# Optimization experiments

Measured on AMD Instinct MI355X. Metric: run time of the kernel, lower is better.

## Reference

```python
import jax, jax.numpy as jnp
import numpy as np

NUM_GRAPHS = 512
NODES_PER_GRAPH = 200  # == N_rois
EDGES_PER_GRAPH = 3200  # avg degree 16
N_ROIS = 200
HIDDEN = 64
OUT = 2


def setup_inputs() -> dict:
    key = jax.random.key(0)
    ks = jax.random.split(key, 7)
    N = NUM_GRAPHS * NODES_PER_GRAPH
    E = NUM_GRAPHS * EDGES_PER_GRAPH
    x = jax.random.normal(ks[0], (N, N_ROIS), dtype=jnp.float32)
    # edges sampled within each graph's node block
    base = jnp.repeat(jnp.arange(NUM_GRAPHS, dtype=jnp.int64) * NODES_PER_GRAPH, EDGES_PER_GRAPH)
    local = jax.random.randint(ks[1], (2, E), 0, NODES_PER_GRAPH, dtype=jnp.int64)
    edge_index = local + base[None, :]
    batch = jnp.arange(N, dtype=jnp.int64) // NODES_PER_GRAPH
    conv_w = jax.random.normal(ks[2], (N_ROIS, HIDDEN), dtype=jnp.float32) * 0.1
    conv_b = jax.random.normal(ks[3], (HIDDEN,), dtype=jnp.float32) * 0.1
    lin_w = jax.random.normal(ks[4], (HIDDEN, OUT), dtype=jnp.float32) * 0.1
    lin_b = jax.random.normal(ks[5], (OUT,), dtype=jnp.float32) * 0.1
    return {"x": x, "edge_index": edge_index, "batch": batch,
            "conv_w": conv_w, "conv_b": conv_b, "lin_w": lin_w, "lin_b": lin_b}


def reference(x, edge_index, batch, conv_w, conv_b, lin_w, lin_b):
    N = x.shape[0]
    # GCNConv: linear transform first (N_rois -> hidden), then normalized aggregation
    h = x @ conv_w  # [N, H]
    loops = jnp.arange(N, dtype=edge_index.dtype)
    src = jnp.concatenate([edge_index[0], loops])  # add self-loops (PyG default)
    dst = jnp.concatenate([edge_index[1], loops])
    deg = jax.ops.segment_sum(jnp.ones_like(dst, dtype=h.dtype), dst, num_segments=N)
    dinv = jnp.where(deg > 0, jax.lax.rsqrt(deg), jnp.zeros_like(deg))
    norm = dinv[src] * dinv[dst]  # D^-1/2 (A+I) D^-1/2 edge weights
    agg = jax.ops.segment_sum(h[src] * norm[:, None], dst, num_segments=N) + conv_b
    hr = jax.nn.relu(agg)
    x_pool = jax.ops.segment_max(hr, batch, num_segments=NUM_GRAPHS)  # [G, H]
    out = x_pool @ lin_w + lin_b  # [G, OUT]
    return out, x_pool
```

## Files before the change

### kernel.cpp

```cpp
#include <hip/hip_runtime.h>

#define NUM_GRAPHS 512
#define NPG 200
#define EPG 3200
#define NROIS 200
#define HID 64
#define OUTC 2
#define NT (NUM_GRAPHS * NPG)
#define APITCH 232
#define HPITCH 232
#define WIMG_ELEMS (7 * 4 * 2 * 64 * 8)
#define WS_NEEDED ((size_t)WIMG_ELEMS * 2 + (size_t)HID * NT * 2)

typedef short v8s __attribute__((ext_vector_type(8)));
typedef float v4f __attribute__((ext_vector_type(4)));

__device__ __forceinline__ unsigned bf16_rne(float f) {
  unsigned u = __float_as_uint(f);
  return (u + 0x7fffu + ((u >> 16) & 1u)) >> 16;
}

__global__ void prep_wimg(const float* __restrict__ cw, unsigned short* __restrict__ wimg) {
  int idx = blockIdx.x * 256 + threadIdx.x;
  if (idx >= WIMG_ELEMS) return;
  int i    = idx & 7;
  int lane = (idx >> 3) & 63;
  int hl   = (idx >> 9) & 1;
  int nt   = (idx >> 10) & 3;
  int kt   = idx >> 12;
  int k  = kt * 32 + (lane >> 4) * 8 + i;
  int ch = nt * 16 + (lane & 15);
  float f = (k < NROIS) ? cw[k * HID + ch] : 0.f;
  unsigned hi = bf16_rne(f);
  float lo = f - __uint_as_float(hi << 16);
  wimg[idx] = hl ? (unsigned short)(__float_as_uint(lo) >> 16) : (unsigned short)hi;
}

struct __align__(16) Smem1 {
  unsigned short xhi[64 * HPITCH];
  unsigned short xlo[64 * HPITCH];
};

__global__ __launch_bounds__(256, 2)
void gcn_gemm1(const float* __restrict__ x,
               const unsigned short* __restrict__ wimg,
               unsigned short* __restrict__ hpT) {
  __shared__ Smem1 s;
  const int tid = threadIdx.x;
  const int blk = blockIdx.x;
  const int lane = tid & 63;
  const int w = __builtin_amdgcn_readfirstlane(tid >> 6);
  const int ml = tid & 15;
  const int q  = (tid >> 4) & 3;

  #pragma unroll
  for (int t = 0; t < 13; ++t) {
    int i = tid + t * 256;
    if (i < 3200) {
      int node = i / 50;
      int kc = (i - node * 50) * 4;
      const float4 v = *(const float4*)(x + (size_t)(blk * 64 + node) * NROIS + kc);
      const float ff[4] = {v.x, v.y, v.z, v.w};
      unsigned hh[4], ll[4];
      #pragma unroll
      for (int e = 0; e < 4; ++e) {
        unsigned u = __float_as_uint(ff[e]);
        hh[e] = u >> 16;
        float lo = ff[e] - __uint_as_float(hh[e] << 16);
        ll[e] = __float_as_uint(lo) >> 16;
      }
      uint2 ph = {hh[0] | (hh[1] << 16), hh[2] | (hh[3] << 16)};
      uint2 pl = {ll[0] | (ll[1] << 16), ll[2] | (ll[3] << 16)};
      *(uint2*)&s.xhi[node * HPITCH + kc] = ph;
      *(uint2*)&s.xlo[node * HPITCH + kc] = pl;
    }
  }
  for (int i = tid; i < 64 * 32; i += 256) {
    int node = i >> 5, c = 200 + (i & 31);
    s.xhi[node * HPITCH + c] = 0;
    s.xlo[node * HPITCH + c] = 0;
  }
  __syncthreads();

  v4f acc[4];
  #pragma unroll
  for (int nt = 0; nt < 4; ++nt) acc[nt] = (v4f){0.f, 0.f, 0.f, 0.f};

  for (int kt = 0; kt < 7; ++kt) {
    const int k0 = kt * 32 + q * 8;
    const v8s xh = *(const v8s*)&s.xhi[(w * 16 + ml) * HPITCH + k0];
    const v8s xl = *(const v8s*)&s.xlo[(w * 16 + ml) * HPITCH + k0];
    #pragma unroll
    for (int nt = 0; nt < 4; ++nt) {
      const unsigned short* pw = wimg + (size_t)(((kt * 4 + nt) * 2) * 64 + lane) * 8;
      const v8s whi = *(const v8s*)pw;
      const v8s wlo = *(const v8s*)(pw + 64 * 8);
      acc[nt] = __builtin_amdgcn_mfma_f32_16x16x32_bf16(whi, xl, acc[nt], 0, 0, 0);
      acc[nt] = __builtin_amdgcn_mfma_f32_16x16x32_bf16(wlo, xh, acc[nt], 0, 0, 0);
      acc[nt] = __builtin_amdgcn_mfma_f32_16x16x32_bf16(whi, xh, acc[nt], 0, 0, 0);
    }
  }

  const int gnode = blk * 64 + w * 16 + ml;
  #pragma unroll
  for (int nt = 0; nt < 4; ++nt) {
    #pragma unroll
    for (int r = 0; r < 4; ++r) {
      const int ch = nt * 16 + q * 4 + r;
      hpT[(size_t)ch * NT + gnode] = (unsigned short)bf16_rne(acc[nt][r]);
    }
  }
}

struct __align__(16) Smem2 {
  unsigned char adj[208 * APITCH];
  unsigned short hpTl[HID * HPITCH];
  float dinv[NPG];
  int cnt[NPG];
  int pool[HID];
};

__global__ __launch_bounds__(512, 4)
void gcn_agg(const int* __restrict__ ei,
             const unsigned short* __restrict__ hpT,
             const float* __restrict__ cb,
             const float* __restrict__ lw,
             const float* __restrict__ lb,
             float* __restrict__ out,
             int Etot) {
  __shared__ Smem2 s;
  const int g = blockIdx.x;
  const int tid = threadIdx.x;
  const int base = g * NPG;
  const int ebase = g * EPG;
  const int lane = tid & 63;
  const int w = __builtin_amdgcn_readfirstlane(tid >> 6);
  const int ml = tid & 15;
  const int q  = (tid >> 4) & 3;

  {
    uint4* z = (uint4*)&s;
    const uint4 z4 = {0u, 0u, 0u, 0u};
    #pragma unroll
    for (int i = 0; i < 10; ++i) {
      int idx = tid + i * 512;
      if (idx < (208 * APITCH + HID * HPITCH * 2) / 16) z[idx] = z4;
    }
    if (tid < NPG) s.cnt[tid] = 0;
    if (tid < HID) s.pool[tid] = 0;
  }
  __syncthreads();

  int esrc[7], edst[7];
  #pragma unroll
  for (int r = 0; r < 7; ++r) {
    int e = tid + r * 512;
    esrc[r] = -1; edst[r] = 0;
    if (e < EPG) {
      esrc[r] = ei[ebase + e] - base;
      edst[r] = ei[Etot + ebase + e] - base;
      atomicAdd(&s.cnt[edst[r]], 1);
    }
  }
  __syncthreads();

  if (tid < NPG) s.dinv[tid] = rsqrtf((float)(s.cnt[tid] + 1));
  __syncthreads();

  {
    unsigned* adjW = (unsigned*)s.adj;
    #pragma unroll
    for (int r = 0; r < 7; ++r) {
      if (esrc[r] >= 0) {
        int idx = edst[r] * APITCH + esrc[r];
        atomicAdd(&adjW[idx >> 2], 1u << ((idx & 3) * 8));
      }
    }
    if (tid < NPG) {
      int idx = tid * APITCH + tid;
      atomicAdd(&adjW[idx >> 2], 1u << ((idx & 3) * 8));
    }
  }

  #pragma unroll
  for (int t = 0; t < 13; ++t) {
    int i = tid + t * 512;
    if (i < HID * 100) {
      int ch = i / 100;
      int c2 = (i - ch * 100) * 2;
      unsigned v = *(const unsigned*)(hpT + (size_t)ch * NT + base + c2);
      float f0 = __uint_as_float(v << 16)         * s.dinv[c2];
      float f1 = __uint_as_float(v & 0xffff0000u) * s.dinv[c2 + 1];
      *(unsigned*)&s.hpTl[ch * HPITCH + c2] = bf16_rne(f0) | (bf16_rne(f1) << 16);
    }
  }
  __syncthreads();

  {
    int mts[2];
    mts[0] = w;
    mts[1] = (w < 5) ? 8 + w : -1;

    v4f acc2[2][4];
    #pragma unroll
    for (int a = 0; a < 2; ++a)
      #pragma unroll
      for (int b = 0; b < 4; ++b)
        acc2[a][b] = (v4f){0.f, 0.f, 0.f, 0.f};

    for (int kt = 0; kt < 7; ++kt) {
      const int k0 = kt * 32 + q * 8;

      v8s bf[4];
      #pragma unroll
      for (int nt = 0; nt < 4; ++nt)
        bf[nt] = *(const v8s*)&s.hpTl[(nt * 16 + ml) * HPITCH + k0];

      #pragma unroll
      for (int mi = 0; mi < 2; ++mi) {
        if (mts[mi] >= 0) {
          const int row = mts[mi] * 16 + ml;
          const uint2 dd = *(const uint2*)&s.adj[row * APITCH + k0];
          v8s af;
          #pragma unroll
          for (int i = 0; i < 4; ++i) {
            af[i]     = (short)(__float_as_uint((float)((dd.x >> (8 * i)) & 0xffu)) >> 16);
            af[i + 4] = (short)(__float_as_uint((float)((dd.y >> (8 * i)) & 0xffu)) >> 16);
          }
          #pragma unroll
          for (int nt = 0; nt < 4; ++nt)
            acc2[mi][nt] = __builtin_amdgcn_mfma_f32_16x16x32_bf16(af, bf[nt], acc2[mi][nt], 0, 0, 0);
        }
      }
    }

    float cbv[4];
    #pragma unroll
    for (int nt = 0; nt < 4; ++nt) cbv[nt] = cb[nt * 16 + ml];
    float mx[4] = {0.f, 0.f, 0.f, 0.f};
    #pragma unroll
    for (int mi = 0; mi < 2; ++mi) {
      if (mts[mi] >= 0) {
        #pragma unroll
        for (int r = 0; r < 4; ++r) {
          const int row = mts[mi] * 16 + q * 4 + r;
          if (row < NPG) {
            const float dv = s.dinv[row];
            #pragma unroll
            for (int nt = 0; nt < 4; ++nt) {
              float v = fmaxf(fmaf(dv, acc2[mi][nt][r], cbv[nt]), 0.f);
              mx[nt] = fmaxf(mx[nt], v);
            }
          }
        }
      }
    }
    #pragma unroll
    for (int nt = 0; nt < 4; ++nt) {
      mx[nt] = fmaxf(mx[nt], __shfl_xor(mx[nt], 16));
      mx[nt] = fmaxf(mx[nt], __shfl_xor(mx[nt], 32));
    }
    if (q == 0 && (lane >> 5) == 0) {
      #pragma unroll
      for (int nt = 0; nt < 4; ++nt)
        atomicMax(&s.pool[nt * 16 + ml], __float_as_int(mx[nt]));
    }
  }
  __syncthreads();

  if (tid < HID) {
    const float xp = __int_as_float(s.pool[tid]);
    out[NUM_GRAPHS * OUTC + g * HID + tid] = xp;
    float p0 = xp * lw[tid * 2 + 0];
    float p1 = xp * lw[tid * 2 + 1];
    #pragma unroll
    for (int off = 32; off > 0; off >>= 1) {
      p0 += __shfl_down(p0, off);
      p1 += __shfl_down(p1, off);
    }
    if (tid == 0) {
      out[g * OUTC + 0] = p0 + lb[0];
      out[g * OUTC + 1] = p1 + lb[1];
    }
  }
}

struct __align__(16) SmemF {
  unsigned char adj[208 * APITCH];
  unsigned short hpT[HID * HPITCH];
  float dinv[NPG];
  int cnt[NPG];
  int pool[HID];
};

__global__ __launch_bounds__(512, 4)
void gcn_fused_fb(const float* __restrict__ x,
                  const int* __restrict__ ei,
                  const float* __restrict__ cw,
                  const float* __restrict__ cb,
                  const float* __restrict__ lw,
                  const float* __restrict__ lb,
                  float* __restrict__ out,
                  int Etot) {
  __shared__ SmemF s;
  const int g = blockIdx.x;
  const int tid = threadIdx.x;
  const int base = g * NPG;
  const int ebase = g * EPG;
  const int lane = tid & 63;
  const int w = __builtin_amdgcn_readfirstlane(tid >> 6);
  const int ml = tid & 15;
  const int q  = (tid >> 4) & 3;

  {
    uint4* z = (uint4*)&s;
    const uint4 z4 = {0u, 0u, 0u, 0u};
    #pragma unroll
    for (int i = 0; i < 10; ++i) {
      int idx = tid + i * 512;
      if (idx < (208 * APITCH + HID * HPITCH * 2) / 16) z[idx] = z4;
    }
    if (tid < NPG) s.cnt[tid] = 0;
    if (tid < HID) s.pool[tid] = 0;
  }
  __syncthreads();

  int esrc[7], edst[7];
  #pragma unroll
  for (int r = 0; r < 7; ++r) {
    int e = tid + r * 512;
    esrc[r] = -1; edst[r] = 0;
    if (e < EPG) {
      esrc[r] = ei[ebase + e] - base;
      edst[r] = ei[Etot + ebase + e] - base;
      atomicAdd(&s.cnt[edst[r]], 1);
    }
  }
  __syncthreads();

  if (tid < NPG) s.dinv[tid] = rsqrtf((float)(s.cnt[tid] + 1));

  {
    unsigned* adjW = (unsigned*)s.adj;
    #pragma unroll
    for (int r = 0; r < 7; ++r) {
      if (esrc[r] >= 0) {
        int idx = edst[r] * APITCH + esrc[r];
        atomicAdd(&adjW[idx >> 2], 1u << ((idx & 3) * 8));
      }
    }
    if (tid < NPG) {
      int idx = tid * APITCH + tid;
      atomicAdd(&adjW[idx >> 2], 1u << ((idx & 3) * 8));
    }
  }
  __syncthreads();

  {
    int mts[2];
    mts[0] = w;
    mts[1] = (w < 5) ? 8 + w : -1;
    v4f acc[2][4];
    #pragma unroll
    for (int a = 0; a < 2; ++a)
      #pragma unroll
      for (int b = 0; b < 4; ++b)
        acc[a][b] = (v4f){0.f, 0.f, 0.f, 0.f};

    for (int kt = 0; kt < 7; ++kt) {
      const int k0 = kt * 32 + q * 8;
      const bool kok = (k0 < NROIS);
      v8s bhi[4], blo[4];
      #pragma unroll
      for (int nt = 0; nt < 4; ++nt) {
        #pragma unroll
        for (int i = 0; i < 8; ++i) {
          float f = kok ? cw[(k0 + i) * HID + nt * 16 + ml] : 0.f;
          unsigned hb = bf16_rne(f);
          float lo = f - __uint_as_float(hb << 16);
          bhi[nt][i] = (short)hb;
          blo[nt][i] = (short)(__float_as_uint(lo) >> 16);
        }
      }
      #pragma unroll
      for (int mi = 0; mi < 2; ++mi) {
        if (mts[mi] >= 0) {
          const int row = mts[mi] * 16 + ml;
          v8s ahi, alo;
          if (kok && row < NPG) {
            const float* px = x + (size_t)(base + row) * NROIS + k0;
            const float4 f0 = *(const float4*)px;
            const float4 f1 = *(const float4*)(px + 4);
            const float ff[8] = {f0.x, f0.y, f0.z, f0.w, f1.x, f1.y, f1.z, f1.w};
            #pragma unroll
            for (int i = 0; i < 8; ++i) {
              unsigned u = __float_as_uint(ff[i]);
              unsigned hb = u >> 16;
              float lo = ff[i] - __uint_as_float(hb << 16);
              ahi[i] = (short)hb;
              alo[i] = (short)(__float_as_uint(lo) >> 16);
            }
          } else {
            #pragma unroll
            for (int i = 0; i < 8; ++i) { ahi[i] = 0; alo[i] = 0; }
          }
          #pragma unroll
          for (int nt = 0; nt < 4; ++nt) {
            acc[mi][nt] = __builtin_amdgcn_mfma_f32_16x16x32_bf16(ahi, blo[nt], acc[mi][nt], 0, 0, 0);
            acc[mi][nt] = __builtin_amdgcn_mfma_f32_16x16x32_bf16(alo, bhi[nt], acc[mi][nt], 0, 0, 0);
            acc[mi][nt] = __builtin_amdgcn_mfma_f32_16x16x32_bf16(ahi, bhi[nt], acc[mi][nt], 0, 0, 0);
          }
        }
      }
    }
    #pragma unroll
    for (int mi = 0; mi < 2; ++mi) {
      if (mts[mi] >= 0) {
        #pragma unroll
        for (int r = 0; r < 4; ++r) {
          const int row = mts[mi] * 16 + q * 4 + r;
          if (row < NPG) {
            const float dv = s.dinv[row];
            #pragma unroll
            for (int nt = 0; nt < 4; ++nt)
              s.hpT[(nt * 16 + ml) * HPITCH + row] =
                  (unsigned short)bf16_rne(dv * acc[mi][nt][r]);
          }
        }
      }
    }
  }
  __syncthreads();

  {
    int mts[2];
    mts[0] = w;
    mts[1] = (w < 5) ? 8 + w : -1;
    v4f acc2[2][4];
    #pragma unroll
    for (int a = 0; a < 2; ++a)
      #pragma unroll
      for (int b = 0; b < 4; ++b)
        acc2[a][b] = (v4f){0.f, 0.f, 0.f, 0.f};

    for (int kt = 0; kt < 7; ++kt) {
      const int k0 = kt * 32 + q * 8;
      v8s bf[4];
      #pragma unroll
      for (int nt = 0; nt < 4; ++nt)
        bf[nt] = *(const v8s*)&s.hpT[(nt * 16 + ml) * HPITCH + k0];
      #pragma unroll
      for (int mi = 0; mi < 2; ++mi) {
        if (mts[mi] >= 0) {
          const int row = mts[mi] * 16 + ml;
          const uint2 dd = *(const uint2*)&s.adj[row * APITCH + k0];
          v8s af;
          #pragma unroll
          for (int i = 0; i < 4; ++i) {
            af[i]     = (short)(__float_as_uint((float)((dd.x >> (8 * i)) & 0xffu)) >> 16);
            af[i + 4] = (short)(__float_as_uint((float)((dd.y >> (8 * i)) & 0xffu)) >> 16);
          }
          #pragma unroll
          for (int nt = 0; nt < 4; ++nt)
            acc2[mi][nt] = __builtin_amdgcn_mfma_f32_16x16x32_bf16(af, bf[nt], acc2[mi][nt], 0, 0, 0);
        }
      }
    }

    float cbv[4];
    #pragma unroll
    for (int nt = 0; nt < 4; ++nt) cbv[nt] = cb[nt * 16 + ml];
    float mx[4] = {0.f, 0.f, 0.f, 0.f};
    #pragma unroll
    for (int mi = 0; mi < 2; ++mi) {
      if (mts[mi] >= 0) {
        #pragma unroll
        for (int r = 0; r < 4; ++r) {
          const int row = mts[mi] * 16 + q * 4 + r;
          if (row < NPG) {
            const float dv = s.dinv[row];
            #pragma unroll
            for (int nt = 0; nt < 4; ++nt) {
              float v = fmaxf(fmaf(dv, acc2[mi][nt][r], cbv[nt]), 0.f);
              mx[nt] = fmaxf(mx[nt], v);
            }
          }
        }
      }
    }
    #pragma unroll
    for (int nt = 0; nt < 4; ++nt) {
      mx[nt] = fmaxf(mx[nt], __shfl_xor(mx[nt], 16));
      mx[nt] = fmaxf(mx[nt], __shfl_xor(mx[nt], 32));
    }
    if (q == 0 && (lane >> 5) == 0) {
      #pragma unroll
      for (int nt = 0; nt < 4; ++nt)
        atomicMax(&s.pool[nt * 16 + ml], __float_as_int(mx[nt]));
    }
  }
  __syncthreads();

  if (tid < HID) {
    const float xp = __int_as_float(s.pool[tid]);
    out[NUM_GRAPHS * OUTC + g * HID + tid] = xp;
    float p0 = xp * lw[tid * 2 + 0];
    float p1 = xp * lw[tid * 2 + 1];
    #pragma unroll
    for (int off = 32; off > 0; off >>= 1) {
      p0 += __shfl_down(p0, off);
      p1 += __shfl_down(p1, off);
    }
    if (tid == 0) {
      out[g * OUTC + 0] = p0 + lb[0];
      out[g * OUTC + 1] = p1 + lb[1];
    }
  }
}

extern "C" void kernel_launch(void* const* d_in, const int* in_sizes, int n_in,
                              void* d_out, int out_size, void* d_ws, size_t ws_size,
                              hipStream_t stream) {
  const float* x  = (const float*)d_in[0];
  const int*   ei = (const int*)d_in[1];
  const float* cw = (const float*)d_in[3];
  const float* cb = (const float*)d_in[4];
  const float* lw = (const float*)d_in[5];
  const float* lb = (const float*)d_in[6];
  const int Etot = in_sizes[1] / 2;

  if (ws_size >= WS_NEEDED) {
    unsigned short* wimg = (unsigned short*)d_ws;
    unsigned short* hpT  = wimg + WIMG_ELEMS;
    prep_wimg<<<(WIMG_ELEMS + 255) / 256, 256, 0, stream>>>(cw, wimg);
    gcn_gemm1<<<NT / 64, 256, 0, stream>>>(x, wimg, hpT);
    gcn_agg<<<NUM_GRAPHS, 512, 0, stream>>>(ei, hpT, cb, lw, lb, (float*)d_out, Etot);
  } else {
    gcn_fused_fb<<<NUM_GRAPHS, 512, 0, stream>>>(x, ei, cw, cb, lw, lb,
                                                 (float*)d_out, Etot);
  }
}
```

Baseline: 167.8 us.

## Fuse feature GEMM into per-graph aggregation kernel, dropping hpT global round trip

Replaces the separate x@W GEMM kernel and the aggregation kernel with one per-graph kernel. It stages x in 64-column chunks into LDS that is unioned with the adjacency/hpT buffers, and computes h with split-bf16 MFMA. It then writes dinv-scaled h straight into LDS for the aggregation MFMA. This removes the global write and read of the bf16 hpT intermediate and one kernel launch, at the cost of more barriers and weight loads per block. The LDS union also lowers the shared memory footprint.

New measurement: 154.5 us. 8.0% less time.

```diff
diff --git a/kernel.cpp b/kernel.cpp
--- a/kernel.cpp
+++ b/kernel.cpp
@@ -6,11 +6,11 @@
 #define NROIS 200
 #define HID 64
 #define OUTC 2
-#define NT (NUM_GRAPHS * NPG)
 #define APITCH 232
 #define HPITCH 232
+#define XPITCH 72
 #define WIMG_ELEMS (7 * 4 * 2 * 64 * 8)
-#define WS_NEEDED ((size_t)WIMG_ELEMS * 2 + (size_t)HID * NT * 2)
+#define WS_NEEDED ((size_t)WIMG_ELEMS * 2)
 
 typedef short v8s __attribute__((ext_vector_type(8)));
 typedef float v4f __attribute__((ext_vector_type(4)));
@@ -36,99 +36,67 @@
   wimg[idx] = hl ? (unsigned short)(__float_as_uint(lo) >> 16) : (unsigned short)hi;
 }
 
-struct __align__(16) Smem1 {
-  unsigned short xhi[64 * HPITCH];
-  unsigned short xlo[64 * HPITCH];
-};
-
-__global__ __launch_bounds__(256, 2)
-void gcn_gemm1(const float* __restrict__ x,
-               const unsigned short* __restrict__ wimg,
-               unsigned short* __restrict__ hpT) {
-  __shared__ Smem1 s;
-  const int tid = threadIdx.x;
-  const int blk = blockIdx.x;
-  const int lane = tid & 63;
-  const int w = __builtin_amdgcn_readfirstlane(tid >> 6);
-  const int ml = tid & 15;
-  const int q  = (tid >> 4) & 3;
-
-  #pragma unroll
-  for (int t = 0; t < 13; ++t) {
-    int i = tid + t * 256;
-    if (i < 3200) {
-      int node = i / 50;
-      int kc = (i - node * 50) * 4;
-      const float4 v = *(const float4*)(x + (size_t)(blk * 64 + node) * NROIS + kc);
-      const float ff[4] = {v.x, v.y, v.z, v.w};
-      unsigned hh[4], ll[4];
-      #pragma unroll
-      for (int e = 0; e < 4; ++e) {
-        unsigned u = __float_as_uint(ff[e]);
-        hh[e] = u >> 16;
-        float lo = ff[e] - __uint_as_float(hh[e] << 16);
-        ll[e] = __float_as_uint(lo) >> 16;
-      }
-      uint2 ph = {hh[0] | (hh[1] << 16), hh[2] | (hh[3] << 16)};
-      uint2 pl = {ll[0] | (ll[1] << 16), ll[2] | (ll[3] << 16)};
-      *(uint2*)&s.xhi[node * HPITCH + kc] = ph;
-      *(uint2*)&s.xlo[node * HPITCH + kc] = pl;
-    }
-  }
-  for (int i = tid; i < 64 * 32; i += 256) {
-    int node = i >> 5, c = 200 + (i & 31);
-    s.xhi[node * HPITCH + c] = 0;
-    s.xlo[node * HPITCH + c] = 0;
-  }
-  __syncthreads();
-
-  v4f acc[4];
-  #pragma unroll
-  for (int nt = 0; nt < 4; ++nt) acc[nt] = (v4f){0.f, 0.f, 0.f, 0.f};
-
-  for (int kt = 0; kt < 7; ++kt) {
-    const int k0 = kt * 32 + q * 8;
-    const v8s xh = *(const v8s*)&s.xhi[(w * 16 + ml) * HPITCH + k0];
-    const v8s xl = *(const v8s*)&s.xlo[(w * 16 + ml) * HPITCH + k0];
-    #pragma unroll
-    for (int nt = 0; nt < 4; ++nt) {
-      const unsigned short* pw = wimg + (size_t)(((kt * 4 + nt) * 2) * 64 + lane) * 8;
-      const v8s whi = *(const v8s*)pw;
-      const v8s wlo = *(const v8s*)(pw + 64 * 8);
-      acc[nt] = __builtin_amdgcn_mfma_f32_16x16x32_bf16(whi, xl, acc[nt], 0, 0, 0);
-      acc[nt] = __builtin_amdgcn_mfma_f32_16x16x32_bf16(wlo, xh, acc[nt], 0, 0, 0);
-      acc[nt] = __builtin_amdgcn_mfma_f32_16x16x32_bf16(whi, xh, acc[nt], 0, 0, 0);
-    }
-  }
-
-  const int gnode = blk * 64 + w * 16 + ml;
-  #pragma unroll
-  for (int nt = 0; nt < 4; ++nt) {
-    #pragma unroll
-    for (int r = 0; r < 4; ++r) {
-      const int ch = nt * 16 + q * 4 + r;
-      hpT[(size_t)ch * NT + gnode] = (unsigned short)bf16_rne(acc[nt][r]);
-    }
-  }
-}
-
-struct __align__(16) Smem2 {
-  unsigned char adj[208 * APITCH];
-  unsigned short hpTl[HID * HPITCH];
+struct __align__(16) SmemU {
+  union {
+    struct {
+      unsigned short xhi[NPG * XPITCH];
+      unsigned short xlo[NPG * XPITCH];
+    } g1;
+    struct {
+      unsigned char adj[208 * APITCH];
+      unsigned short hpTl[HID * HPITCH];
+    } g2;
+  } u;
   float dinv[NPG];
   int cnt[NPG];
   int pool[HID];
 };
 
+__device__ __forceinline__ void stage_x(SmemU& s, const float* __restrict__ x,
+                                        int base, int tk, int tid) {
+  const int c0 = tk * 64;
+  #pragma unroll
+  for (int r = 0; r < 7; ++r) {
+    int idx = tid + r * 512;
+    if (idx < NPG * 16) {
+      int node = idx >> 4;
+      int f4 = idx & 15;
+      int col = c0 + f4 * 4;
+      float ff[4];
+      if (col + 4 <= NROIS) {
+        const float4 v = *(const float4*)(x + (size_t)(base + node) * NROIS + col);
+        ff[0] = v.x; ff[1] = v.y; ff[2] = v.z; ff[3] = v.w;
+      } else {
+        #pragma unroll
+        for (int e = 0; e < 4; ++e)
+          ff[e] = (col + e < NROIS) ? x[(size_t)(base + node) * NROIS + col + e] : 0.f;
+      }
+      unsigned hh[4], ll[4];
+      #pragma unroll
+      for (int e = 0; e < 4; ++e) {
+        unsigned uu = __float_as_uint(ff[e]);
+        hh[e] = uu >> 16;
+        float lo = ff[e] - __uint_as_float(hh[e] << 16);
+        ll[e] = __float_as_uint(lo) >> 16;
+      }
+      uint2 ph = {hh[0] | (hh[1] << 16), hh[2] | (hh[3] << 16)};
+      uint2 pl = {ll[0] | (ll[1] << 16), ll[2] | (ll[3] << 16)};
+      *(uint2*)&s.u.g1.xhi[node * XPITCH + f4 * 4] = ph;
+      *(uint2*)&s.u.g1.xlo[node * XPITCH + f4 * 4] = pl;
+    }
+  }
+}
+
 __global__ __launch_bounds__(512, 4)
-void gcn_agg(const int* __restrict__ ei,
-             const unsigned short* __restrict__ hpT,
-             const float* __restrict__ cb,
-             const float* __restrict__ lw,
-             const float* __restrict__ lb,
-             float* __restrict__ out,
-             int Etot) {
-  __shared__ Smem2 s;
+void gcn_fused2(const float* __restrict__ x,
+                const int* __restrict__ ei,
+                const unsigned short* __restrict__ wimg,
+                const float* __restrict__ cb,
+                const float* __restrict__ lw,
+                const float* __restrict__ lb,
+                float* __restrict__ out,
+                int Etot) {
+  __shared__ SmemU s;
   const int g = blockIdx.x;
   const int tid = threadIdx.x;
   const int base = g * NPG;
@@ -138,17 +106,8 @@
   const int ml = tid & 15;
   const int q  = (tid >> 4) & 3;
 
-  {
-    uint4* z = (uint4*)&s;
-    const uint4 z4 = {0u, 0u, 0u, 0u};
-    #pragma unroll
-    for (int i = 0; i < 10; ++i) {
-      int idx = tid + i * 512;
-      if (idx < (208 * APITCH + HID * HPITCH * 2) / 16) z[idx] = z4;
-    }
-    if (tid < NPG) s.cnt[tid] = 0;
-    if (tid < HID) s.pool[tid] = 0;
-  }
+  if (tid < NPG) s.cnt[tid] = 0;
+  if (tid < HID) s.pool[tid] = 0;
   __syncthreads();
 
   int esrc[7], edst[7];
@@ -162,13 +121,89 @@
       atomicAdd(&s.cnt[edst[r]], 1);
     }
   }
+  stage_x(s, x, base, 0, tid);
   __syncthreads();
 
   if (tid < NPG) s.dinv[tid] = rsqrtf((float)(s.cnt[tid] + 1));
-  __syncthreads();
-
-  {
-    unsigned* adjW = (unsigned*)s.adj;
+
+  int mts[2];
+  mts[0] = w;
+  mts[1] = (w < 5) ? 8 + w : -1;
+
+  v4f acc[2][4];
+  #pragma unroll
+  for (int a = 0; a < 2; ++a)
+    #pragma unroll
+    for (int b = 0; b < 4; ++b)
+      acc[a][b] = (v4f){0.f, 0.f, 0.f, 0.f};
+
+  for (int tk = 0; tk < 4; ++tk) {
+    #pragma unroll
+    for (int half = 0; half < 2; ++half) {
+      const int kt = tk * 2 + half;
+      if (kt < 7) {
+        const int koff = half * 32 + q * 8;
+        v8s whi[4], wlo[4];
+        #pragma unroll
+        for (int nt = 0; nt < 4; ++nt) {
+          const unsigned short* pw = wimg + (size_t)(((kt * 4 + nt) * 2) * 64 + lane) * 8;
+          whi[nt] = *(const v8s*)pw;
+          wlo[nt] = *(const v8s*)(pw + 64 * 8);
+        }
+        #pragma unroll
+        for (int mi = 0; mi < 2; ++mi) {
+          if (mts[mi] >= 0) {
+            const int node = mts[mi] * 16 + ml;
+            const int nrd = (node < NPG) ? node : 0;
+            const v8s xh = *(const v8s*)&s.u.g1.xhi[nrd * XPITCH + koff];
+            const v8s xl = *(const v8s*)&s.u.g1.xlo[nrd * XPITCH + koff];
+            #pragma unroll
+            for (int nt = 0; nt < 4; ++nt) {
+              acc[mi][nt] = __builtin_amdgcn_mfma_f32_16x16x32_bf16(whi[nt], xl, acc[mi][nt], 0, 0, 0);
+              acc[mi][nt] = __builtin_amdgcn_mfma_f32_16x16x32_bf16(wlo[nt], xh, acc[mi][nt], 0, 0, 0);
+              acc[mi][nt] = __builtin_amdgcn_mfma_f32_16x16x32_bf16(whi[nt], xh, acc[mi][nt], 0, 0, 0);
+            }
+          }
+        }
+      }
+    }
+    __syncthreads();
+    if (tk < 3) {
+      stage_x(s, x, base, tk + 1, tid);
+      __syncthreads();
+    }
+  }
+
+  {
+    uint4* z = (uint4*)&s.u;
+    const uint4 z4 = {0u, 0u, 0u, 0u};
+    #pragma unroll
+    for (int i = 0; i < 10; ++i) {
+      int idx = tid + i * 512;
+      if (idx < (208 * APITCH + HID * HPITCH * 2) / 16) z[idx] = z4;
+    }
+  }
+  __syncthreads();
+
+  #pragma unroll
+  for (int mi = 0; mi < 2; ++mi) {
+    if (mts[mi] >= 0) {
+      const int node = mts[mi] * 16 + ml;
+      if (node < NPG) {
+        const float dv = s.dinv[node];
+        #pragma unroll
+        for (int nt = 0; nt < 4; ++nt) {
+          #pragma unroll
+          for (int r = 0; r < 4; ++r) {
+            const int ch = nt * 16 + q * 4 + r;
+            s.u.g2.hpTl[ch * HPITCH + node] = (unsigned short)bf16_rne(dv * acc[mi][nt][r]);
+          }
+        }
+      }
+    }
+  }
+  {
+    unsigned* adjW = (unsigned*)s.u.g2.adj;
     #pragma unroll
     for (int r = 0; r < 7; ++r) {
       if (esrc[r] >= 0) {
@@ -181,26 +216,9 @@
       atomicAdd(&adjW[idx >> 2], 1u << ((idx & 3) * 8));
     }
   }
-
-  #pragma unroll
-  for (int t = 0; t < 13; ++t) {
-    int i = tid + t * 512;
-    if (i < HID * 100) {
-      int ch = i / 100;
-      int c2 = (i - ch * 100) * 2;
-      unsigned v = *(const unsigned*)(hpT + (size_t)ch * NT + base + c2);
-      float f0 = __uint_as_float(v << 16)         * s.dinv[c2];
-      float f1 = __uint_as_float(v & 0xffff0000u) * s.dinv[c2 + 1];
-      *(unsigned*)&s.hpTl[ch * HPITCH + c2] = bf16_rne(f0) | (bf16_rne(f1) << 16);
-    }
-  }
-  __syncthreads();
-
-  {
-    int mts[2];
-    mts[0] = w;
-    mts[1] = (w < 5) ? 8 + w : -1;
-
+  __syncthreads();
+
+  {
     v4f acc2[2][4];
     #pragma unroll
     for (int a = 0; a < 2; ++a)
@@ -214,13 +232,13 @@
       v8s bf[4];
       #pragma unroll
       for (int nt = 0; nt < 4; ++nt)
-        bf[nt] = *(const v8s*)&s.hpTl[(nt * 16 + ml) * HPITCH + k0];
+        bf[nt] = *(const v8s*)&s.u.g2.hpTl[(nt * 16 + ml) * HPITCH + k0];
 
       #pragma unroll
       for (int mi = 0; mi < 2; ++mi) {
         if (mts[mi] >= 0) {
           const int row = mts[mi] * 16 + ml;
-          const uint2 dd = *(const uint2*)&s.adj[row * APITCH + k0];
+          const uint2 dd = *(const uint2*)&s.u.g2.adj[row * APITCH + k0];
           v8s af;
           #pragma unroll
           for (int i = 0; i < 4; ++i) {
@@ -531,10 +549,9 @@
 
   if (ws_size >= WS_NEEDED) {
     unsigned short* wimg = (unsigned short*)d_ws;
-    unsigned short* hpT  = wimg + WIMG_ELEMS;
     prep_wimg<<<(WIMG_ELEMS + 255) / 256, 256, 0, stream>>>(cw, wimg);
-    gcn_gemm1<<<NT / 64, 256, 0, stream>>>(x, wimg, hpT);
-    gcn_agg<<<NUM_GRAPHS, 512, 0, stream>>>(ei, hpT, cb, lw, lb, (float*)d_out, Etot);
+    gcn_fused2<<<NUM_GRAPHS, 512, 0, stream>>>(x, ei, wimg, cb, lw, lb,
+                                               (float*)d_out, Etot);
   } else {
     gcn_fused_fb<<<NUM_GRAPHS, 512, 0, stream>>>(x, ei, cw, cb, lw, lb,
                                                  (float*)d_out, Etot);
```
